# Kernel tuning notes

Measured on AMD Instinct MI355X. Metric: run time of the kernel, lower is better.

Reference implementation:

```python
import jax, jax.numpy as jnp
import numpy as np

G = 8
K = 3  # kernel size; Unfold uses padding=1, stride=1 -> output same HxW


def _unfold3x3(x):
    # x: (b, c, h, w) -> (b, c, K*K, h, w), patch order (kh, kw) matching torch Unfold
    b, c, h, w = x.shape
    xp = jnp.pad(x, ((0, 0), (0, 0), (1, 1), (1, 1)))
    patches = [xp[:, :, i:i + h, j:j + w] for i in range(K) for j in range(K)]
    return jnp.stack(patches, axis=2)


def setup_inputs() -> dict:
    key = jax.random.key(0)
    k1, k2, k3, k4, k5 = jax.random.split(key, 5)
    b, c, h, w = 16, 256, 56, 56
    r = 2
    return {
        "x": jax.random.normal(k1, (b, c, h, w), dtype=jnp.float32),
        "w_reduce": jax.random.normal(k2, (c // r, c), dtype=jnp.float32) * (1.0 / np.sqrt(c)),
        "b_reduce": jax.random.normal(k3, (c // r,), dtype=jnp.float32) * 0.01,
        "w_span": jax.random.normal(k4, (K * K * G, c // r), dtype=jnp.float32) * (1.0 / np.sqrt(c // r)),
        "b_span": jax.random.normal(k5, (K * K * G,), dtype=jnp.float32) * 0.01,
    }


def reference(x, w_reduce, b_reduce, w_span, b_span):
    b, c, h, w = x.shape
    kk = K * K
    # dynamic kernel: two 1x1 convs (ss=1 -> no pooling)
    red = jnp.einsum('bchw,oc->bohw', x, w_reduce) + b_reduce[None, :, None, None]
    ker = jnp.einsum('bohw,ko->bkhw', red, w_span) + b_span[None, :, None, None]
    ker = ker.reshape(b, G, kk, h, w)
    # unfold: (b, c, kk, h, w) -> (b, G, c//G, kk, h, w)
    xu = _unfold3x3(x).reshape(b, G, c // G, kk, h, w)
    # broadcast-mul and reduce over kernel positions
    out = jnp.einsum('bgkhw,bgdkhw->bgdhw', ker, xu)
    return out.reshape(b, c, h, w)
```

## Files before the change

### kernel.cpp

```cpp
#include <hip/hip_runtime.h>
#include <hip/hip_bf16.h>

#define HW 3136
#define CC 256
#define MM 72
#define HH 56
#define WW 56

typedef __attribute__((ext_vector_type(8))) short short8;
typedef __attribute__((ext_vector_type(4))) float f32x4;

#define WAITVM(n) asm volatile("s_waitcnt vmcnt(" #n ")" ::: "memory")

__device__ __forceinline__ void blockbar() {
    asm volatile("" ::: "memory");
    __builtin_amdgcn_s_barrier();
    asm volatile("" ::: "memory");
}

__device__ inline unsigned short f2b(float f) {
    unsigned u; __builtin_memcpy(&u, &f, 4);
    unsigned r = u + 0x7fffu + ((u >> 16) & 1u);
    return (unsigned short)(r >> 16);
}
__device__ inline float b2f(unsigned short s) {
    unsigned u = ((unsigned)s) << 16; float f; __builtin_memcpy(&f, &u, 4);
    return f;
}
__device__ __forceinline__ unsigned short f2b_native(float f) {
    __hip_bfloat16 h = __float2bfloat16(f);
    unsigned short s; __builtin_memcpy(&s, &h, 2);
    return s;
}

__device__ __forceinline__ void gl2lds16(const float* g, float* l) {
    __builtin_amdgcn_global_load_lds(
        (const __attribute__((address_space(1))) void*)g,
        (__attribute__((address_space(3))) void*)l, 16, 0, 0);
}

__global__ __launch_bounds__(256) void k0_combine(
    const float* __restrict__ w_reduce,
    const float* __restrict__ b_reduce,
    const float* __restrict__ w_span,
    const float* __restrict__ b_span,
    unsigned short* __restrict__ wbf,
    float* __restrict__ bcomb)
{
    __shared__ float red[4][64];
    __shared__ float redb[256];

    const int m  = blockIdx.x;
    const int cq = blockIdx.y;
    const int t  = threadIdx.x;
    const int oq = t >> 6;
    const int cl = t & 63;
    const int c  = cq * 64 + cl;

    float acc = 0.f;
    if (m < MM) {
        const float* wsB = w_span   + m * 128 + oq * 32;
        const float* wrB = w_reduce + (size_t)(oq * 32) * 256 + c;
#pragma unroll 8
        for (int o = 0; o < 32; ++o)
            acc = fmaf(wsB[o], wrB[(size_t)o * 256], acc);
    }
    if (oq != 0) red[oq][cl] = acc;
    __syncthreads();
    if (oq == 0)
        wbf[m * 256 + c] = f2b(acc + red[1][cl] + red[2][cl] + red[3][cl]);

    if (cq == 0) {
        redb[t] = (m < MM && t < 128) ? w_span[m * 128 + t] * b_reduce[t] : 0.f;
        __syncthreads();
#pragma unroll
        for (int s2 = 128; s2 > 0; s2 >>= 1) {
            if (t < s2) redb[t] += redb[t + s2];
            __syncthreads();
        }
        if (t == 0) bcomb[m] = (m < MM ? b_span[m] : 0.f) + redb[0];
    }
}

__global__ __launch_bounds__(448, 4) void k_fused(
    const float* __restrict__ x,
    const unsigned short* __restrict__ wbf,
    const float* __restrict__ bcomb,
    float* __restrict__ out)
{
    __shared__ __align__(16) float xsb[3 * 3584];
    __shared__ __align__(16) unsigned short wsl[3][2560];
    __shared__ __align__(16) unsigned short kl[MM * 112];

    const int L   = blockIdx.x;
    const int wk  = (L & 7) * 56 + (L >> 3);
    const int b   = wk / 28;
    const int rem = wk - b * 28;
    const int ht  = rem >> 1;
    const int cs  = rem & 1;
    const int h0  = ht * 4;
    const int c0  = cs * 28;

    const int t    = threadIdx.x;
    const int lane = t & 63;
    const int wv   = t >> 6;
    const int l15  = lane & 15;
    const int q    = lane >> 4;

    const int chh   = t / 28;
    const int rem28 = t - chh * 28;
    const int rA    = rem28 / 7;
    const int qA    = rem28 - rA * 7;

    const float* xb = x + (size_t)b * CC * HW;

    const int nb   = wv * 16 + l15;
    const int nb2  = q * 112 + nb;
    const int swA  = (l15 ^ (l15 >> 2)) & 3;
    const int aBo  = l15 * 32 + (q ^ swA) * 8;
    const int cA   = ((chh & 3) << 3) | (chh >> 2);
    const int pxo  = (h0 + rA) * WW + c0 + qA * 4;
    const int wswr = ((t >> 2) ^ (t >> 4)) & 3;
    const unsigned short* wsrc0 = wbf + (t >> 2) * 256 + ((t & 3) ^ wswr) * 8;

    int boff[2];
#pragma unroll
    for (int i = 0; i < 2; ++i) {
        const int f  = i * 448 + t;
        const int fc = f < 864 ? f : 863;
        const int d  = fc / 54;
        const int r2 = fc - d * 54;
        const int rr = r2 / 9;
        const int qd = r2 - rr * 9;
        const int hh = h0 - 1 + rr;
        const int hc = hh < 0 ? 0 : (hh > 55 ? 55 : hh);
        int colc = c0 - 4 + qd * 4;
        colc = colc < 0 ? 0 : (colc > 52 ? 52 : colc);
        boff[i] = d * HW + hc * WW + colc;
    }

    float vmm[3];
#pragma unroll
    for (int kh = 0; kh < 3; ++kh) {
        const int row = h0 + rA - 1 + kh;
        vmm[kh] = (row >= 0 && row < HH) ? 1.f : 0.f;
    }
    const float lm  = (cs == 0 && qA == 0) ? 0.f : 1.f;
    const float rmm = (cs == 1 && qA == 6) ? 0.f : 1.f;

    auto stageX = [&](int s) {
        const float* sp = xb + (size_t)(s * 32 + cA) * HW + pxo;
        float* dp = xsb + (s % 3) * 3584 + t * 4;
        gl2lds16(sp, dp);
        gl2lds16(sp + (size_t)4 * HW, dp + 1792);
    };
    auto stageW = [&](int s) {
        if (t < 320)
            gl2lds16((const float*)(wsrc0 + s * 32), (float*)(wsl[s % 3]) + t * 4);
    };
    auto stageB = [&](int c) {
        const float* gp = xb + (size_t)(c * 16) * HW;
        float* dp = xsb + ((8 + c) % 3) * 3584;
        gl2lds16(gp + boff[0], dp + t * 4);
        gl2lds16(gp + boff[1], dp + (448 + t) * 4);
    };

    f32x4 acc[5];
#pragma unroll
    for (int mt = 0; mt < 5; ++mt)
#pragma unroll
        for (int r = 0; r < 4; ++r)
            acc[mt][r] = bcomb[mt * 16 + q * 4 + r];

    stageX(0); stageW(0);
    stageX(1); stageW(1);

#pragma unroll 1
    for (int p = 0; p < 8; ++p) {
        if (p < 7) { if (t < 320) WAITVM(3); else WAITVM(2); }
        else       { WAITVM(2); }
        blockbar();
        if (p < 6)       { stageX(p + 2); stageW(p + 2); }
        else if (p == 6) { stageB(0); }
        else             { stageB(1); }

        const float* bufA = xsb + (p % 3) * 3584;
        const unsigned short* wp = wsl[p % 3];
        union { short8 v; unsigned short u16[8]; } bq;
#pragma unroll
        for (int j = 0; j < 8; ++j)
            bq.u16[j] = f2b_native(bufA[nb2 + j * 448]);
#pragma unroll
        for (int mt = 0; mt < 5; ++mt) {
            const short8 aq = *(const short8*)&wp[mt * 512 + aBo];
            acc[mt] = __builtin_amdgcn_mfma_f32_16x16x32_bf16(aq, bq.v, acc[mt], 0, 0, 0);
        }
        if (p == 7) {
#pragma unroll
            for (int mt = 0; mt < 5; ++mt)
#pragma unroll
                for (int r = 0; r < 4; ++r) {
                    const int m = mt * 16 + q * 4 + r;
                    if (m < MM) kl[m * 112 + nb] = f2b(acc[mt][r]);
                }
            asm volatile("s_waitcnt lgkmcnt(0)" ::: "memory");
        }
    }

    f32x4 kr[9];
#pragma unroll 1
    for (int g2 = 0; g2 < 16; ++g2) {
        if (g2 == 0)       WAITVM(2);
        else if (g2 <= 14) WAITVM(3);
        else               WAITVM(1);
        blockbar();
        if (g2 <= 13) stageB(g2 + 2);

        if ((g2 & 1) == 0) {
            const int g = g2 >> 1;
            ushort4 krb[9];
#pragma unroll
            for (int kk = 0; kk < 9; ++kk)
                krb[kk] = *(const ushort4*)&kl[(g * 9 + kk) * 112 + rA * 28 + qA * 4];
#pragma unroll
            for (int kh = 0; kh < 3; ++kh) {
#pragma unroll
                for (int j = 0; j < 3; ++j) {
                    const int kk = kh * 3 + j;
                    kr[kk].x = b2f(krb[kk].x) * vmm[kh];
                    kr[kk].y = b2f(krb[kk].y) * vmm[kh];
                    kr[kk].z = b2f(krb[kk].z) * vmm[kh];
                    kr[kk].w = b2f(krb[kk].w) * vmm[kh];
                }
                kr[kh * 3 + 0].x *= lm;
                kr[kh * 3 + 2].w *= rmm;
            }
        }

        const float* bp = xsb + ((8 + g2) % 3) * 3584 + chh * 216;
        f32x4 a = {0.f, 0.f, 0.f, 0.f};
#pragma unroll
        for (int kh = 0; kh < 3; ++kh) {
            const float* rowp = bp + (rA + kh) * 36;
            const f32x4 q0v = *(const f32x4*)(rowp + qA * 4);
            const f32x4 q1v = *(const f32x4*)(rowp + qA * 4 + 4);
            const float tl  = rowp[qA * 4 + 8];
            const float w0 = q0v.w, w1 = q1v.x, w2 = q1v.y,
                        w3 = q1v.z, w4 = q1v.w, w5 = tl;
            const f32x4 k0v = kr[kh * 3 + 0];
            const f32x4 k1v = kr[kh * 3 + 1];
            const f32x4 k2v = kr[kh * 3 + 2];
            a.x = fmaf(k0v.x, w0, a.x); a.y = fmaf(k0v.y, w1, a.y);
            a.z = fmaf(k0v.z, w2, a.z); a.w = fmaf(k0v.w, w3, a.w);
            a.x = fmaf(k1v.x, w1, a.x); a.y = fmaf(k1v.y, w2, a.y);
            a.z = fmaf(k1v.z, w3, a.z); a.w = fmaf(k1v.w, w4, a.w);
            a.x = fmaf(k2v.x, w2, a.x); a.y = fmaf(k2v.y, w3, a.y);
            a.z = fmaf(k2v.z, w4, a.z); a.w = fmaf(k2v.w, w5, a.w);
        }
        float* ob = out + ((size_t)b * CC + g2 * 16 + chh) * HW
                  + (h0 + rA) * WW + c0 + qA * 4;
        *(f32x4*)ob = a;
    }
}

extern "C" void kernel_launch(void* const* d_in, const int* in_sizes, int n_in,
                              void* d_out, int out_size, void* d_ws, size_t ws_size,
                              hipStream_t stream) {
    const float* x        = (const float*)d_in[0];
    const float* w_reduce = (const float*)d_in[1];
    const float* b_reduce = (const float*)d_in[2];
    const float* w_span   = (const float*)d_in[3];
    const float* b_span   = (const float*)d_in[4];
    float* out = (float*)d_out;

    char* ws = (char*)d_ws;
    unsigned short* wbf   = (unsigned short*)ws;
    float*          bcomb = (float*)(ws + 40960);

    k0_combine<<<dim3(80, 4), 256, 0, stream>>>(w_reduce, b_reduce, w_span, b_span,
                                                wbf, bcomb);
    k_fused<<<dim3(448), 448, 0, stream>>>(x, wbf, bcomb, out);
}
```

Measured before the change: 37.88 us.

## Split fused kernel into GEMM kernel and apply kernel with doubled grid

The single fused kernel, which computed the dynamic 3x3 kernels by MFMA and then applied them, is split into two launches. The first writes the bf16 dynamic kernels per tile to workspace. The second runs 896 blocks, each handling half the channel groups, with smaller LDS and a higher occupancy bound. This aims for more parallelism and occupancy in the memory-bound apply phase, at the cost of an extra launch, a global round-trip for the kernel tensor, and x being read again.

```diff
diff --git a/kernel.cpp b/kernel.cpp
--- a/kernel.cpp
+++ b/kernel.cpp
@@ -82,15 +82,14 @@
     }
 }
 
-__global__ __launch_bounds__(448, 4) void k_fused(
+__global__ __launch_bounds__(448, 4) void kA_gemm(
     const float* __restrict__ x,
     const unsigned short* __restrict__ wbf,
     const float* __restrict__ bcomb,
-    float* __restrict__ out)
+    unsigned short* __restrict__ kerb2)
 {
     __shared__ __align__(16) float xsb[3 * 3584];
     __shared__ __align__(16) unsigned short wsl[3][2560];
-    __shared__ __align__(16) unsigned short kl[MM * 112];
 
     const int L   = blockIdx.x;
     const int wk  = (L & 7) * 56 + (L >> 3);
@@ -100,6 +99,7 @@
     const int cs  = rem & 1;
     const int h0  = ht * 4;
     const int c0  = cs * 28;
+    const int tile = b * 28 + ht * 2 + cs;
 
     const int t    = threadIdx.x;
     const int lane = t & 63;
@@ -122,6 +122,84 @@
     const int pxo  = (h0 + rA) * WW + c0 + qA * 4;
     const int wswr = ((t >> 2) ^ (t >> 4)) & 3;
     const unsigned short* wsrc0 = wbf + (t >> 2) * 256 + ((t & 3) ^ wswr) * 8;
+
+    auto stageX = [&](int s) {
+        const float* sp = xb + (size_t)(s * 32 + cA) * HW + pxo;
+        float* dp = xsb + (s % 3) * 3584 + t * 4;
+        gl2lds16(sp, dp);
+        gl2lds16(sp + (size_t)4 * HW, dp + 1792);
+    };
+    auto stageW = [&](int s) {
+        if (t < 320)
+            gl2lds16((const float*)(wsrc0 + s * 32), (float*)(wsl[s % 3]) + t * 4);
+    };
+
+    f32x4 acc[5];
+#pragma unroll
+    for (int mt = 0; mt < 5; ++mt)
+#pragma unroll
+        for (int r = 0; r < 4; ++r)
+            acc[mt][r] = bcomb[mt * 16 + q * 4 + r];
+
+    stageX(0); stageW(0);
+    stageX(1); stageW(1);
+
+#pragma unroll 1
+    for (int p = 0; p < 8; ++p) {
+        if (p < 7) { if (t < 320) WAITVM(3); else WAITVM(2); }
+        else       { WAITVM(0); }
+        blockbar();
+        if (p < 6) { stageX(p + 2); stageW(p + 2); }
+
+        const float* bufA = xsb + (p % 3) * 3584;
+        const unsigned short* wp = wsl[p % 3];
+        union { short8 v; unsigned short u16[8]; } bq;
+#pragma unroll
+        for (int j = 0; j < 8; ++j)
+            bq.u16[j] = f2b_native(bufA[nb2 + j * 448]);
+#pragma unroll
+        for (int mt = 0; mt < 5; ++mt) {
+            const short8 aq = *(const short8*)&wp[mt * 512 + aBo];
+            acc[mt] = __builtin_amdgcn_mfma_f32_16x16x32_bf16(aq, bq.v, acc[mt], 0, 0, 0);
+        }
+    }
+
+    unsigned short* kt = kerb2 + (size_t)tile * 8064;
+#pragma unroll
+    for (int mt = 0; mt < 5; ++mt)
+#pragma unroll
+        for (int r = 0; r < 4; ++r) {
+            const int m = mt * 16 + q * 4 + r;
+            if (m < MM) kt[m * 112 + nb] = f2b(acc[mt][r]);
+        }
+}
+
+__global__ __launch_bounds__(448, 7) void kB_apply(
+    const float* __restrict__ x,
+    const unsigned short* __restrict__ kerb2,
+    float* __restrict__ out)
+{
+    __shared__ __align__(16) float xsb[2 * 3584];
+    __shared__ __align__(16) unsigned short klb[36 * 112];
+
+    const int L   = blockIdx.x;
+    const int wk  = (L & 7) * 112 + (L >> 3);
+    const int b   = wk / 56;
+    int r2d = wk - b * 56;
+    const int ht  = r2d >> 2;
+    const int cs  = (r2d >> 1) & 1;
+    const int hv  = r2d & 1;
+    const int h0  = ht * 4;
+    const int c0  = cs * 28;
+    const int tile = b * 28 + ht * 2 + cs;
+
+    const int t    = threadIdx.x;
+    const int chh   = t / 28;
+    const int rem28 = t - chh * 28;
+    const int rA    = rem28 / 7;
+    const int qA    = rem28 - rA * 7;
+
+    const float* xb = x + (size_t)b * CC * HW;
 
     int boff[2];
 #pragma unroll
@@ -148,80 +226,33 @@
     const float lm  = (cs == 0 && qA == 0) ? 0.f : 1.f;
     const float rmm = (cs == 1 && qA == 6) ? 0.f : 1.f;
 
-    auto stageX = [&](int s) {
-        const float* sp = xb + (size_t)(s * 32 + cA) * HW + pxo;
-        float* dp = xsb + (s % 3) * 3584 + t * 4;
-        gl2lds16(sp, dp);
-        gl2lds16(sp + (size_t)4 * HW, dp + 1792);
-    };
-    auto stageW = [&](int s) {
-        if (t < 320)
-            gl2lds16((const float*)(wsrc0 + s * 32), (float*)(wsl[s % 3]) + t * 4);
-    };
     auto stageB = [&](int c) {
-        const float* gp = xb + (size_t)(c * 16) * HW;
-        float* dp = xsb + ((8 + c) % 3) * 3584;
+        const float* gp = xb + (size_t)(hv * 128 + c * 16) * HW;
+        float* dp = xsb + (c & 1) * 3584;
         gl2lds16(gp + boff[0], dp + t * 4);
         gl2lds16(gp + boff[1], dp + (448 + t) * 4);
     };
 
-    f32x4 acc[5];
-#pragma unroll
-    for (int mt = 0; mt < 5; ++mt)
-#pragma unroll
-        for (int r = 0; r < 4; ++r)
-            acc[mt][r] = bcomb[mt * 16 + q * 4 + r];
-
-    stageX(0); stageW(0);
-    stageX(1); stageW(1);
-
+    const float* ksf = (const float*)(kerb2 + (size_t)tile * 8064 + hv * 4032);
+    float* kld = (float*)klb;
+    gl2lds16(ksf + t * 4, kld + t * 4);
+    if (t < 56) gl2lds16(ksf + (448 + t) * 4, kld + (448 + t) * 4);
+    stageB(0);
+
+    f32x4 kr[9];
 #pragma unroll 1
     for (int p = 0; p < 8; ++p) {
-        if (p < 7) { if (t < 320) WAITVM(3); else WAITVM(2); }
-        else       { WAITVM(2); }
+        if (p == 0) WAITVM(0);
+        else        WAITVM(1);
         blockbar();
-        if (p < 6)       { stageX(p + 2); stageW(p + 2); }
-        else if (p == 6) { stageB(0); }
-        else             { stageB(1); }
-
-        const float* bufA = xsb + (p % 3) * 3584;
-        const unsigned short* wp = wsl[p % 3];
-        union { short8 v; unsigned short u16[8]; } bq;
-#pragma unroll
-        for (int j = 0; j < 8; ++j)
-            bq.u16[j] = f2b_native(bufA[nb2 + j * 448]);
-#pragma unroll
-        for (int mt = 0; mt < 5; ++mt) {
-            const short8 aq = *(const short8*)&wp[mt * 512 + aBo];
-            acc[mt] = __builtin_amdgcn_mfma_f32_16x16x32_bf16(aq, bq.v, acc[mt], 0, 0, 0);
-        }
-        if (p == 7) {
-#pragma unroll
-            for (int mt = 0; mt < 5; ++mt)
-#pragma unroll
-                for (int r = 0; r < 4; ++r) {
-                    const int m = mt * 16 + q * 4 + r;
-                    if (m < MM) kl[m * 112 + nb] = f2b(acc[mt][r]);
-                }
-            asm volatile("s_waitcnt lgkmcnt(0)" ::: "memory");
-        }
-    }
-
-    f32x4 kr[9];
-#pragma unroll 1
-    for (int g2 = 0; g2 < 16; ++g2) {
-        if (g2 == 0)       WAITVM(2);
-        else if (g2 <= 14) WAITVM(3);
-        else               WAITVM(1);
-        blockbar();
-        if (g2 <= 13) stageB(g2 + 2);
-
-        if ((g2 & 1) == 0) {
-            const int g = g2 >> 1;
+        if (p < 7) stageB(p + 1);
+
+        if ((p & 1) == 0) {
+            const int gl = p >> 1;
             ushort4 krb[9];
 #pragma unroll
             for (int kk = 0; kk < 9; ++kk)
-                krb[kk] = *(const ushort4*)&kl[(g * 9 + kk) * 112 + rA * 28 + qA * 4];
+                krb[kk] = *(const ushort4*)&klb[(gl * 9 + kk) * 112 + rA * 28 + qA * 4];
 #pragma unroll
             for (int kh = 0; kh < 3; ++kh) {
 #pragma unroll
@@ -237,7 +268,7 @@
             }
         }
 
-        const float* bp = xsb + ((8 + g2) % 3) * 3584 + chh * 216;
+        const float* bp = xsb + (p & 1) * 3584 + chh * 216;
         f32x4 a = {0.f, 0.f, 0.f, 0.f};
 #pragma unroll
         for (int kh = 0; kh < 3; ++kh) {
@@ -257,7 +288,7 @@
             a.x = fmaf(k2v.x, w2, a.x); a.y = fmaf(k2v.y, w3, a.y);
             a.z = fmaf(k2v.z, w4, a.z); a.w = fmaf(k2v.w, w5, a.w);
         }
-        float* ob = out + ((size_t)b * CC + g2 * 16 + chh) * HW
+        float* ob = out + ((size_t)b * CC + hv * 128 + p * 16 + chh) * HW
                   + (h0 + rA) * WW + c0 + qA * 4;
         *(f32x4*)ob = a;
     }
@@ -276,8 +307,10 @@
     char* ws = (char*)d_ws;
     unsigned short* wbf   = (unsigned short*)ws;
     float*          bcomb = (float*)(ws + 40960);
+    unsigned short* kerb2 = (unsigned short*)(ws + 41472);
 
     k0_combine<<<dim3(80, 4), 256, 0, stream>>>(w_reduce, b_reduce, w_span, b_span,
                                                 wbf, bcomb);
-    k_fused<<<dim3(448), 448, 0, stream>>>(x, wbf, bcomb, out);
-}
+    kA_gemm<<<dim3(448), 448, 0, stream>>>(x, wbf, bcomb, kerb2);
+    kB_apply<<<dim3(896), 448, 0, stream>>>(x, kerb2, out);
+}
```

Result: slower. 42.83 us (+13.1%).
